# Kernel optimization log

Measured on AMD Instinct MI355X. Metric: run time of the kernel, lower is better.

The kernel has to match this reference:

```python
import jax, jax.numpy as jnp
import numpy as np

BLOCK_SIZE = 16
THRESH = 0.1


def _hadamard(n: int) -> np.ndarray:
    # Sylvester construction, matches WHTBlock.generate_walsh_matrix
    H = np.ones((1, 1), dtype=np.float32)
    while H.shape[0] < n:
        H = np.block([[H, H], [H, -H]])
    return H.astype(np.float32)


def setup_inputs() -> dict:
    key = jax.random.key(0)
    x = jax.random.normal(key, (32, 3, 1024, 1024), dtype=jnp.float32)
    return {"input": x}


def reference(input) -> jnp.ndarray:
    b, c, h, w = input.shape
    bs = BLOCK_SIZE
    # reflect-pad H, W up to a multiple of block_size (no-op when divisible)
    h_pad = (h + bs - 1) // bs * bs - h
    w_pad = (w + bs - 1) // bs * bs - w
    x = jnp.pad(input, ((0, 0), (0, 0), (0, h_pad), (0, w_pad)), mode="reflect")
    hn, wn = x.shape[-2:]
    # unfold into non-overlapping blocks: [b, c, nh, nw, bs, bs]
    x = x.reshape(b, c, hn // bs, bs, wn // bs, bs).transpose(0, 1, 2, 4, 3, 5)
    # normalized Hadamard: H / sqrt(n)
    Hn = jnp.asarray(_hadamard(bs)) / np.sqrt(np.float32(bs))
    # 2D WHT = Hn @ block @ Hn.T (H is symmetric but we keep the transposes explicit)
    x = jnp.einsum("bcnmij,kj->bcnmik", x, Hn)   # rows of each block: x @ Hn.T
    x = jnp.einsum("li,bcnmij->bcnmlj", Hn, x)   # cols of each block: Hn @ x
    # threshold: zero small-magnitude coefficients
    out = jnp.where(jnp.abs(x) < THRESH, jnp.zeros((), x.dtype), x)
    return out
```

## Files before the change

### kernel.cpp

```cpp
#include <hip/hip_runtime.h>

#define THRESH 0.1f

__global__ __launch_bounds__(256) void wht16_kernel(const float* __restrict__ in,
                                                    float* __restrict__ out) {
    const int g = blockIdx.x * 256 + threadIdx.x;
    const int lane = g & 63;
    const int strip = g >> 6;
    const int p = strip >> 10;
    const int rem = strip & 1023;
    const int i = rem >> 4;
    const int j4 = rem & 15;

    const long long in_base = (long long)p * 1048576
                            + (long long)(i * 16) * 1024
                            + (long long)(j4 * 64 + lane);
    float v[16];
#pragma unroll
    for (int r = 0; r < 16; ++r)
        v[r] = in[in_base + (long long)r * 1024];

#pragma unroll
    for (int m = 1; m < 16; m <<= 1) {
#pragma unroll
        for (int r = 0; r < 16; ++r) {
            if (!(r & m)) {
                const float a = v[r];
                const float b = v[r | m];
                v[r]     = a + b;
                v[r | m] = a - b;
            }
        }
    }

#pragma unroll
    for (int m = 1; m < 16; m <<= 1) {
        const bool upper = (lane & m) != 0;
#pragma unroll
        for (int r = 0; r < 16; ++r) {
            const float partner = __shfl_xor(v[r], m, 64);
            v[r] = upper ? (partner - v[r]) : (v[r] + partner);
        }
    }

    const int j = j4 * 4 + (lane >> 4);
    const long long out_base = ((long long)((p * 64 + i) * 64 + j)) * 256 + (lane & 15);
#pragma unroll
    for (int r = 0; r < 16; ++r) {
        float x = v[r] * 0.0625f;
        if (fabsf(x) < THRESH) x = 0.0f;
        out[out_base + r * 16] = x;
    }
}

extern "C" void kernel_launch(void* const* d_in, const int* in_sizes, int n_in,
                              void* d_out, int out_size, void* d_ws, size_t ws_size,
                              hipStream_t stream) {
    const float* in = (const float*)d_in[0];
    float* out = (float*)d_out;
    const long long n = (long long)in_sizes[0];
    const int total_threads = (int)(n / 16);
    const int blocks = total_threads / 256;
    wht16_kernel<<<blocks, 256, 0, stream>>>(in, out);
}
```

Baseline: 623.9 us.

## Vectorize WHT16 with float4 per thread, cutting cross-lane shuffles

Each thread now loads four adjacent columns as float4 across 16 rows, so it handles 64 elements instead of 16. Two of the four column butterfly stages now run in registers, leaving two shuffle stages, done with fmaf and a sign multiply. Stores become float4 writes, and the launch uses a fixed block count of 6144. The aim is fewer memory instructions and fewer shuffles for this bandwidth-bound kernel, at the cost of higher register use per thread, fewer waves in flight, and a grid size hardcoded to this input shape.

After: 640.3 us. 2.6% more time.

```diff
diff --git a/kernel.cpp b/kernel.cpp
--- a/kernel.cpp
+++ b/kernel.cpp
@@ -4,52 +4,78 @@
 
 __global__ __launch_bounds__(256) void wht16_kernel(const float* __restrict__ in,
                                                     float* __restrict__ out) {
-    const int g = blockIdx.x * 256 + threadIdx.x;
-    const int lane = g & 63;
-    const int strip = g >> 6;
-    const int p = strip >> 10;
-    const int rem = strip & 1023;
-    const int i = rem >> 4;
-    const int j4 = rem & 15;
+    const int wave = (blockIdx.x << 2) + (threadIdx.x >> 6);
+    const int lane = threadIdx.x & 63;
+    const int s = wave & 3;
+    const int i = (wave >> 2) & 63;
+    const int p = wave >> 8;
 
-    const long long in_base = (long long)p * 1048576
-                            + (long long)(i * 16) * 1024
-                            + (long long)(j4 * 64 + lane);
-    float v[16];
+    const float* src = in + (size_t)p * 1048576 + (size_t)(i * 16) * 1024
+                          + s * 256 + lane * 4;
+
+    float v[16][4];
 #pragma unroll
-    for (int r = 0; r < 16; ++r)
-        v[r] = in[in_base + (long long)r * 1024];
+    for (int r = 0; r < 16; ++r) {
+        const float4 t = *reinterpret_cast<const float4*>(src + (size_t)r * 1024);
+        v[r][0] = t.x; v[r][1] = t.y; v[r][2] = t.z; v[r][3] = t.w;
+    }
 
 #pragma unroll
     for (int m = 1; m < 16; m <<= 1) {
 #pragma unroll
         for (int r = 0; r < 16; ++r) {
             if (!(r & m)) {
-                const float a = v[r];
-                const float b = v[r | m];
-                v[r]     = a + b;
-                v[r | m] = a - b;
+#pragma unroll
+                for (int k = 0; k < 4; ++k) {
+                    const float a = v[r][k];
+                    const float b = v[r | m][k];
+                    v[r][k]     = a + b;
+                    v[r | m][k] = a - b;
+                }
             }
         }
     }
 
 #pragma unroll
-    for (int m = 1; m < 16; m <<= 1) {
-        const bool upper = (lane & m) != 0;
+    for (int r = 0; r < 16; ++r) {
+        float a, b;
+        a = v[r][0]; b = v[r][1]; v[r][0] = a + b; v[r][1] = a - b;
+        a = v[r][2]; b = v[r][3]; v[r][2] = a + b; v[r][3] = a - b;
+        a = v[r][0]; b = v[r][2]; v[r][0] = a + b; v[r][2] = a - b;
+        a = v[r][1]; b = v[r][3]; v[r][1] = a + b; v[r][3] = a - b;
+    }
+
+    const float s1 = (lane & 1) ? -1.0f : 1.0f;
+    const float s2 = (lane & 2) ? -1.0f : 1.0f;
 #pragma unroll
-        for (int r = 0; r < 16; ++r) {
-            const float partner = __shfl_xor(v[r], m, 64);
-            v[r] = upper ? (partner - v[r]) : (v[r] + partner);
+    for (int r = 0; r < 16; ++r) {
+#pragma unroll
+        for (int k = 0; k < 4; ++k) {
+            const float pa = __shfl_xor(v[r][k], 1, 64);
+            v[r][k] = fmaf(s1, v[r][k], pa);
+        }
+    }
+#pragma unroll
+    for (int r = 0; r < 16; ++r) {
+#pragma unroll
+        for (int k = 0; k < 4; ++k) {
+            const float pa = __shfl_xor(v[r][k], 2, 64);
+            v[r][k] = fmaf(s2, v[r][k], pa);
         }
     }
 
-    const int j = j4 * 4 + (lane >> 4);
-    const long long out_base = ((long long)((p * 64 + i) * 64 + j)) * 256 + (lane & 15);
+    const int j = (s << 4) + (lane >> 2);
+    float4* dst = reinterpret_cast<float4*>(out)
+                + ((size_t)((p * 64 + i) * 64 + j) << 6) + (lane & 3);
 #pragma unroll
     for (int r = 0; r < 16; ++r) {
-        float x = v[r] * 0.0625f;
-        if (fabsf(x) < THRESH) x = 0.0f;
-        out[out_base + r * 16] = x;
+        float4 o;
+        float x;
+        x = v[r][0] * 0.0625f; o.x = (fabsf(x) < THRESH) ? 0.0f : x;
+        x = v[r][1] * 0.0625f; o.y = (fabsf(x) < THRESH) ? 0.0f : x;
+        x = v[r][2] * 0.0625f; o.z = (fabsf(x) < THRESH) ? 0.0f : x;
+        x = v[r][3] * 0.0625f; o.w = (fabsf(x) < THRESH) ? 0.0f : x;
+        dst[r * 4] = o;
     }
 }
 
@@ -58,8 +84,6 @@
                               hipStream_t stream) {
     const float* in = (const float*)d_in[0];
     float* out = (float*)d_out;
-    const long long n = (long long)in_sizes[0];
-    const int total_threads = (int)(n / 16);
-    const int blocks = total_threads / 256;
+    const int blocks = 6144;
     wht16_kernel<<<blocks, 256, 0, stream>>>(in, out);
 }
```
